# Kernel tuning notes

Hardware: AMD Instinct MI355X
Metric: run time of the kernel (lower is better)

The kernel has to match this reference:

```python
import jax, jax.numpy as jnp
import numpy as np

B, S, W = 32, 256, 32
T = 16               # topics per doc, each spanning L = S//T sentences
VOCAB, E, H, D = 400001, 300, 128, 128


def _gru_scan(x, Wih, Whh, bih, bhh, reverse=False):
    """x: [B,S,E] -> (outputs [B,S,H], final hidden [B,H]). Torch GRU cell math."""
    h0 = jnp.zeros((x.shape[0], Whh.shape[1]), x.dtype)
    gi_all = jnp.einsum('bse,ge->bsg', x, Wih) + bih  # precompute input gates [B,S,3H]

    def step(h, gi):
        gh = h @ Whh.T + bhh
        ir, iz, inn = jnp.split(gi, 3, axis=-1)
        hr, hz, hn = jnp.split(gh, 3, axis=-1)
        r = jax.nn.sigmoid(ir + hr)
        z = jax.nn.sigmoid(iz + hz)
        n = jnp.tanh(inn + r * hn)
        h_new = (1.0 - z) * n + z * h
        return h_new, h_new

    hT, hs = jax.lax.scan(step, h0, jnp.swapaxes(gi_all, 0, 1), reverse=reverse)
    return jnp.swapaxes(hs, 0, 1), hT


def setup_inputs() -> dict:
    key = jax.random.key(0)
    ks = jax.random.split(key, 16)
    sc_i = 1.0 / np.sqrt(H)
    L = S // T
    starts = (jnp.arange(T, dtype=jnp.int32) * L + 1)          # 1-based inclusive
    ends = (jnp.arange(T, dtype=jnp.int32) + 1) * L
    tse = jnp.broadcast_to(jnp.stack([starts, ends], axis=-1)[None], (B, T, 2)).astype(jnp.int32)
    return {
        'word_ids': jax.random.randint(ks[0], (B, S, W), 0, VOCAB, dtype=jnp.int32),
        'topic_start_ends': tse,
        'embed_table': jax.random.normal(ks[1], (VOCAB, E), jnp.float32) * 0.6,
        'Wih_f': jax.random.normal(ks[2], (3 * H, E), jnp.float32) * sc_i,
        'Whh_f': jax.random.normal(ks[3], (3 * H, H), jnp.float32) * sc_i,
        'bih_f': jax.random.normal(ks[4], (3 * H,), jnp.float32) * sc_i,
        'bhh_f': jax.random.normal(ks[5], (3 * H,), jnp.float32) * sc_i,
        'Wih_b': jax.random.normal(ks[6], (3 * H, E), jnp.float32) * sc_i,
        'Whh_b': jax.random.normal(ks[7], (3 * H, H), jnp.float32) * sc_i,
        'bih_b': jax.random.normal(ks[8], (3 * H,), jnp.float32) * sc_i,
        'bhh_b': jax.random.normal(ks[9], (3 * H,), jnp.float32) * sc_i,
        'v_attention': jax.random.normal(ks[10], (4 * H, 1), jnp.float32),
        'W_attention': jax.random.normal(ks[11], (4 * H, 4 * H), jnp.float32) * (1.0 / np.sqrt(4 * H)),
        'W1': jax.random.normal(ks[12], (D, 4 * H), jnp.float32) * (1.0 / np.sqrt(4 * H)),
        'b1': jax.random.normal(ks[13], (D,), jnp.float32) * 0.01,
        'W2': jax.random.normal(ks[14], (1, D), jnp.float32) * (1.0 / np.sqrt(D)),
        'b2': jax.random.normal(ks[15], (1,), jnp.float32) * 0.01,
    }


def reference(word_ids, topic_start_ends, embed_table,
              Wih_f, Whh_f, bih_f, bhh_f, Wih_b, Whh_b, bih_b, bhh_b,
              v_attention, W_attention, W1, b1, W2, b2):
    b, s, _ = word_ids.shape
    h = Whh_f.shape[1]
    # --- sent_encoder: gather word embeddings, mean-pool per sentence ---
    sent_emb = jnp.mean(embed_table[word_ids], axis=2)          # [B,S,E]
    # --- doc_encoder: bi-GRU ---
    out_f, hT_f = _gru_scan(sent_emb, Wih_f, Whh_f, bih_f, bhh_f, reverse=False)
    out_b, hT_b = _gru_scan(sent_emb, Wih_b, Whh_b, bih_b, bhh_b, reverse=True)
    sent_rep = jnp.concatenate([out_f, out_b], axis=-1)         # [B,S,2H]
    # faithful to hidden.view(batch_size, 2H) on hidden of shape [2,B,H]
    doc_vec = jnp.stack([hT_f, hT_b], axis=0).reshape(b, 2 * h)
    doc_rep = jnp.broadcast_to(doc_vec[:, None, :], (b, s, 2 * h))
    # topic reps via segment difference of cumulative GRU states (pad trick)
    pad = jnp.pad(sent_rep, ((0, 0), (1, 1), (0, 0)))           # [B,S+2,2H]
    starts = topic_start_ends[:, :, 0]                          # [B,T], 1-based
    ends = topic_start_ends[:, :, 1]

    def gat(idx, lo, hi):
        return jnp.take_along_axis(pad[..., lo:hi], idx[:, :, None], axis=1)
    fwd_part = gat(ends, 0, h) - gat(starts - 1, 0, h)
    bwd_part = gat(starts, h, 2 * h) - gat(ends + 1, h, 2 * h)
    topic_mat = jnp.concatenate([fwd_part, bwd_part], axis=-1)  # [B,T,2H]
    # scatter topic vectors to sentences: topic id = #starts at or before sentence
    sidx = jnp.arange(s, dtype=starts.dtype)
    topic_id = jnp.sum(sidx[None, :, None] >= (starts - 1)[:, None, :], axis=-1) - 1  # [B,S]
    topic_rep = jnp.take_along_axis(topic_mat, topic_id[:, :, None], axis=1)          # [B,S,2H]
    # --- decoder ---
    cat_ds = jnp.concatenate([doc_rep, sent_rep], axis=-1)      # [B,S,4H]
    cat_ts = jnp.concatenate([topic_rep, sent_rep], axis=-1)
    doc_scores = jnp.tanh(cat_ds @ W_attention) @ v_attention   # [B,S,1]
    topic_scores = jnp.tanh(cat_ts @ W_attention) @ v_attention
    doc_w = jax.nn.softmax(doc_scores, axis=1)
    topic_w = jax.nn.softmax(topic_scores, axis=1)
    context = doc_w * doc_rep + topic_w * topic_rep             # [B,S,2H]
    inp = jnp.concatenate([sent_rep, context], axis=-1)         # [B,S,4H]
    hdd = jax.nn.relu(inp @ W1.T + b1)                          # dropout = identity (eval)
    logits = (hdd @ W2.T + b2).squeeze(-1)                      # [B,S]
    return logits
```

## Files before the change

kernel.cpp:

```cpp
#include <hip/hip_runtime.h>
#include <hip/hip_bf16.h>
#include <cstdint>

#define Bk 32
#define Sk 256
#define Wk 32
#define Tk 16
#define Ek 300
#define Hk 128
#define Dk 128
#define NROWS (Bk*Sk)
#define GI_N  (3*Hk*2)

__device__ __forceinline__ float fast_sigmoid(float x) {
    return 1.f / (1.f + __expf(-x));
}
__device__ __forceinline__ float fast_tanh(float x) {
    float ax = fabsf(x);
    float e = __expf(2.f * ax);
    float t = 1.f - 2.f / (1.f + e);
    return copysignf(t, x);
}
__device__ __forceinline__ void barrier_lgkm() {
    asm volatile("s_waitcnt lgkmcnt(0)" ::: "memory");
    __builtin_amdgcn_s_barrier();
}
__device__ __forceinline__ void fma44(const float4& a, const float4& b, float (&c)[4][4]) {
    c[0][0]=fmaf(a.x,b.x,c[0][0]); c[0][1]=fmaf(a.x,b.y,c[0][1]); c[0][2]=fmaf(a.x,b.z,c[0][2]); c[0][3]=fmaf(a.x,b.w,c[0][3]);
    c[1][0]=fmaf(a.y,b.x,c[1][0]); c[1][1]=fmaf(a.y,b.y,c[1][1]); c[1][2]=fmaf(a.y,b.z,c[1][2]); c[1][3]=fmaf(a.y,b.w,c[1][3]);
    c[2][0]=fmaf(a.z,b.x,c[2][0]); c[2][1]=fmaf(a.z,b.y,c[2][1]); c[2][2]=fmaf(a.z,b.z,c[2][2]); c[2][3]=fmaf(a.z,b.w,c[2][3]);
    c[3][0]=fmaf(a.w,b.x,c[3][0]); c[3][1]=fmaf(a.w,b.y,c[3][1]); c[3][2]=fmaf(a.w,b.z,c[3][2]); c[3][3]=fmaf(a.w,b.w,c[3][3]);
}

__global__ __launch_bounds__(256) void pack_kernel(
    const float* __restrict__ Wf, const float* __restrict__ Wb,
    const float* __restrict__ bf, const float* __restrict__ bb,
    const float* __restrict__ W1,
    float* __restrict__ Bgi, float* __restrict__ bias_gi, float* __restrict__ BW1)
{
    int idx = blockIdx.x * 256 + threadIdx.x;
    if (idx < 300 * 768) {
        int k = idx / 768, n = idx % 768;
        Bgi[idx] = (n < 384) ? Wf[n * 300 + k] : Wb[(n - 384) * 300 + k];
    }
    if (idx < 768) bias_gi[idx] = (idx < 384) ? bf[idx] : bb[idx - 384];
    if (idx < 512 * 128) {
        int k = idx >> 7, n = idx & 127;
        BW1[idx] = W1[n * 512 + k];
    }
}

__global__ __launch_bounds__(256) void embed_mean_kernel(
    const int* __restrict__ wids, const float* __restrict__ table,
    float* __restrict__ sent_emb)
{
    int wv = (blockIdx.x << 2) + (threadIdx.x >> 6);
    int lane = threadIdx.x & 63;
    if (wv >= NROWS) return;
    const int* idp = wids + (size_t)wv * Wk;
    float4 a0 = {0,0,0,0}, a1 = {0,0,0,0};
    #pragma unroll 4
    for (int w = 0; w < Wk; ++w) {
        int id = idp[w];
        const float4* r4 = reinterpret_cast<const float4*>(table + (size_t)id * Ek);
        float4 v0 = r4[lane];
        a0.x += v0.x; a0.y += v0.y; a0.z += v0.z; a0.w += v0.w;
        if (lane < 11) {
            float4 v1 = r4[64 + lane];
            a1.x += v1.x; a1.y += v1.y; a1.z += v1.z; a1.w += v1.w;
        }
    }
    const float sc = 1.f / 32.f;
    float4* o4 = reinterpret_cast<float4*>(sent_emb + (size_t)wv * Ek);
    float4 o0 = {a0.x*sc, a0.y*sc, a0.z*sc, a0.w*sc};
    o4[lane] = o0;
    if (lane < 11) {
        float4 o1 = {a1.x*sc, a1.y*sc, a1.z*sc, a1.w*sc};
        o4[64 + lane] = o1;
    }
}

template<bool BIAS, bool RELU>
__global__ __launch_bounds__(256) void gemm_kernel(
    const float* __restrict__ A, const float* __restrict__ B,
    const float* __restrict__ bias, float* __restrict__ C,
    int M, int N, int K)
{
    __shared__ float As[64][68];
    __shared__ float Bs[64][68];
    const int tid = threadIdx.x;
    const int m0 = blockIdx.x * 64;
    const int n0 = blockIdx.y * 64;
    const int tx = tid & 15, ty = tid >> 4;
    const int lr = tid >> 2;
    const int lc = tid & 3;
    float acc[4][4] = {};

    for (int k0 = 0; k0 < K; k0 += 64) {
        #pragma unroll
        for (int i = 0; i < 4; ++i) {
            int kk = lc * 4 + i * 16;
            int gm = m0 + lr;
            int gk = k0 + kk;
            float4 v = {0,0,0,0};
            if (gm < M && gk < K)
                v = *reinterpret_cast<const float4*>(A + (size_t)gm * K + gk);
            As[kk+0][lr] = v.x; As[kk+1][lr] = v.y; As[kk+2][lr] = v.z; As[kk+3][lr] = v.w;
        }
        #pragma unroll
        for (int i = 0; i < 4; ++i) {
            int nn = lc * 4 + i * 16;
            int gk = k0 + lr;
            float4 v = {0,0,0,0};
            if (gk < K)
                v = *reinterpret_cast<const float4*>(B + (size_t)gk * N + n0 + nn);
            *reinterpret_cast<float4*>(&Bs[lr][nn]) = v;
        }
        __syncthreads();
        #pragma unroll 8
        for (int k = 0; k < 64; ++k) {
            float4 av = *reinterpret_cast<const float4*>(&As[k][ty*4]);
            float4 bv = *reinterpret_cast<const float4*>(&Bs[k][tx*4]);
            fma44(av, bv, acc);
        }
        __syncthreads();
    }
    #pragma unroll
    for (int r = 0; r < 4; ++r) {
        int row = m0 + ty * 4 + r;
        if (row < M) {
            float4 v = {acc[r][0], acc[r][1], acc[r][2], acc[r][3]};
            if (BIAS) {
                const float* bp = bias + n0 + tx * 4;
                v.x += bp[0]; v.y += bp[1]; v.z += bp[2]; v.w += bp[3];
            }
            if (RELU) {
                v.x = fmaxf(v.x, 0.f); v.y = fmaxf(v.y, 0.f);
                v.z = fmaxf(v.z, 0.f); v.w = fmaxf(v.w, 0.f);
            }
            *reinterpret_cast<float4*>(C + (size_t)row * N + n0 + tx * 4) = v;
        }
    }
}

__global__ __launch_bounds__(512, 1) void gru_scan_kernel(
    const float* __restrict__ gi,
    const float* __restrict__ Whh_f, const float* __restrict__ Whh_b,
    const float* __restrict__ bhh_f, const float* __restrict__ bhh_b,
    float* __restrict__ sent_rep,
    float* __restrict__ hT)
{
    const int blk = blockIdx.x;
    const int dir = blk >> 5;
    const int b   = blk & 31;
    const int t = threadIdx.x;
    const int lane = t & 63;
    const int w_id = t >> 6;
    const int q = lane >> 4;
    const int m = lane & 15;
    const int j = w_id * 16 + m;
    const float* Whh = dir ? Whh_b : Whh_f;
    const float* bhh = dir ? bhh_b : bhh_f;
    __shared__ float hbufA[144];
    __shared__ float hbufB[144];

    const float* wr0 = Whh + (size_t)j * 128 + 32 * q;
    const float* wr1 = wr0 + 128 * 128;
    const float* wr2 = wr0 + 256 * 128;
    float4 wA0 = *reinterpret_cast<const float4*>(wr0 +  0);
    float4 wA1 = *reinterpret_cast<const float4*>(wr0 +  4);
    float4 wA2 = *reinterpret_cast<const float4*>(wr0 +  8);
    float4 wA3 = *reinterpret_cast<const float4*>(wr0 + 12);
    float4 wA4 = *reinterpret_cast<const float4*>(wr0 + 16);
    float4 wA5 = *reinterpret_cast<const float4*>(wr0 + 20);
    float4 wA6 = *reinterpret_cast<const float4*>(wr0 + 24);
    float4 wA7 = *reinterpret_cast<const float4*>(wr0 + 28);
    float4 wB0 = *reinterpret_cast<const float4*>(wr1 +  0);
    float4 wB1 = *reinterpret_cast<const float4*>(wr1 +  4);
    float4 wB2 = *reinterpret_cast<const float4*>(wr1 +  8);
    float4 wB3 = *reinterpret_cast<const float4*>(wr1 + 12);
    float4 wB4 = *reinterpret_cast<const float4*>(wr1 + 16);
    float4 wB5 = *reinterpret_cast<const float4*>(wr1 + 20);
    float4 wB6 = *reinterpret_cast<const float4*>(wr1 + 24);
    float4 wB7 = *reinterpret_cast<const float4*>(wr1 + 28);
    float4 wC0 = *reinterpret_cast<const float4*>(wr2 +  0);
    float4 wC1 = *reinterpret_cast<const float4*>(wr2 +  4);
    float4 wC2 = *reinterpret_cast<const float4*>(wr2 +  8);
    float4 wC3 = *reinterpret_cast<const float4*>(wr2 + 12);
    float4 wC4 = *reinterpret_cast<const float4*>(wr2 + 16);
    float4 wC5 = *reinterpret_cast<const float4*>(wr2 + 20);
    float4 wC6 = *reinterpret_cast<const float4*>(wr2 + 24);
    float4 wC7 = *reinterpret_cast<const float4*>(wr2 + 28);
    const float br = bhh[j];
    const float bz = bhh[128 + j];
    const float bn = bhh[256 + j];

    if (t < 144) { hbufA[t] = 0.f; hbufB[t] = 0.f; }

    const int ji = 36 * (j >> 5) + (j & 31);
    const float* gbase = gi + (size_t)(b * Sk) * GI_N + dir * 384 + j;
    float hold = 0.f;
    float gir = 0.f, giz = 0.f, gin_ = 0.f;
    {
        const int s0 = dir ? (Sk - 1) : 0;
        const float* gp = gbase + (size_t)s0 * GI_N;
        gir = gp[0]; giz = gp[128]; gin_ = gp[256];
    }
    __syncthreads();

    #define STEP(RD, WR, SEXPR) { \
        const int s = (SEXPR); \
        const float4* hseg = reinterpret_cast<const float4*>(RD) + 9 * q; \
        float pA = 0.f, pB = 0.f, pC = 0.f; \
        { float4 h4; \
          h4 = hseg[0]; \
          pA=fmaf(wA0.x,h4.x,pA); pA=fmaf(wA0.y,h4.y,pA); pA=fmaf(wA0.z,h4.z,pA); pA=fmaf(wA0.w,h4.w,pA); \
          pB=fmaf(wB0.x,h4.x,pB); pB=fmaf(wB0.y,h4.y,pB); pB=fmaf(wB0.z,h4.z,pB); pB=fmaf(wB0.w,h4.w,pB); \
          pC=fmaf(wC0.x,h4.x,pC); pC=fmaf(wC0.y,h4.y,pC); pC=fmaf(wC0.z,h4.z,pC); pC=fmaf(wC0.w,h4.w,pC); \
          h4 = hseg[1]; \
          pA=fmaf(wA1.x,h4.x,pA); pA=fmaf(wA1.y,h4.y,pA); pA=fmaf(wA1.z,h4.z,pA); pA=fmaf(wA1.w,h4.w,pA); \
          pB=fmaf(wB1.x,h4.x,pB); pB=fmaf(wB1.y,h4.y,pB); pB=fmaf(wB1.z,h4.z,pB); pB=fmaf(wB1.w,h4.w,pB); \
          pC=fmaf(wC1.x,h4.x,pC); pC=fmaf(wC1.y,h4.y,pC); pC=fmaf(wC1.z,h4.z,pC); pC=fmaf(wC1.w,h4.w,pC); \
          h4 = hseg[2]; \
          pA=fmaf(wA2.x,h4.x,pA); pA=fmaf(wA2.y,h4.y,pA); pA=fmaf(wA2.z,h4.z,pA); pA=fmaf(wA2.w,h4.w,pA); \
          pB=fmaf(wB2.x,h4.x,pB); pB=fmaf(wB2.y,h4.y,pB); pB=fmaf(wB2.z,h4.z,pB); pB=fmaf(wB2.w,h4.w,pB); \
          pC=fmaf(wC2.x,h4.x,pC); pC=fmaf(wC2.y,h4.y,pC); pC=fmaf(wC2.z,h4.z,pC); pC=fmaf(wC2.w,h4.w,pC); \
          h4 = hseg[3]; \
          pA=fmaf(wA3.x,h4.x,pA); pA=fmaf(wA3.y,h4.y,pA); pA=fmaf(wA3.z,h4.z,pA); pA=fmaf(wA3.w,h4.w,pA); \
          pB=fmaf(wB3.x,h4.x,pB); pB=fmaf(wB3.y,h4.y,pB); pB=fmaf(wB3.z,h4.z,pB); pB=fmaf(wB3.w,h4.w,pB); \
          pC=fmaf(wC3.x,h4.x,pC); pC=fmaf(wC3.y,h4.y,pC); pC=fmaf(wC3.z,h4.z,pC); pC=fmaf(wC3.w,h4.w,pC); \
          h4 = hseg[4]; \
          pA=fmaf(wA4.x,h4.x,pA); pA=fmaf(wA4.y,h4.y,pA); pA=fmaf(wA4.z,h4.z,pA); pA=fmaf(wA4.w,h4.w,pA); \
          pB=fmaf(wB4.x,h4.x,pB); pB=fmaf(wB4.y,h4.y,pB); pB=fmaf(wB4.z,h4.z,pB); pB=fmaf(wB4.w,h4.w,pB); \
          pC=fmaf(wC4.x,h4.x,pC); pC=fmaf(wC4.y,h4.y,pC); pC=fmaf(wC4.z,h4.z,pC); pC=fmaf(wC4.w,h4.w,pC); \
          h4 = hseg[5]; \
          pA=fmaf(wA5.x,h4.x,pA); pA=fmaf(wA5.y,h4.y,pA); pA=fmaf(wA5.z,h4.z,pA); pA=fmaf(wA5.w,h4.w,pA); \
          pB=fmaf(wB5.x,h4.x,pB); pB=fmaf(wB5.y,h4.y,pB); pB=fmaf(wB5.z,h4.z,pB); pB=fmaf(wB5.w,h4.w,pB); \
          pC=fmaf(wC5.x,h4.x,pC); pC=fmaf(wC5.y,h4.y,pC); pC=fmaf(wC5.z,h4.z,pC); pC=fmaf(wC5.w,h4.w,pC); \
          h4 = hseg[6]; \
          pA=fmaf(wA6.x,h4.x,pA); pA=fmaf(wA6.y,h4.y,pA); pA=fmaf(wA6.z,h4.z,pA); pA=fmaf(wA6.w,h4.w,pA); \
          pB=fmaf(wB6.x,h4.x,pB); pB=fmaf(wB6.y,h4.y,pB); pB=fmaf(wB6.z,h4.z,pB); pB=fmaf(wB6.w,h4.w,pB); \
          pC=fmaf(wC6.x,h4.x,pC); pC=fmaf(wC6.y,h4.y,pC); pC=fmaf(wC6.z,h4.z,pC); pC=fmaf(wC6.w,h4.w,pC); \
          h4 = hseg[7]; \
          pA=fmaf(wA7.x,h4.x,pA); pA=fmaf(wA7.y,h4.y,pA); pA=fmaf(wA7.z,h4.z,pA); pA=fmaf(wA7.w,h4.w,pA); \
          pB=fmaf(wB7.x,h4.x,pB); pB=fmaf(wB7.y,h4.y,pB); pB=fmaf(wB7.z,h4.z,pB); pB=fmaf(wB7.w,h4.w,pB); \
          pC=fmaf(wC7.x,h4.x,pC); pC=fmaf(wC7.y,h4.y,pC); pC=fmaf(wC7.z,h4.z,pC); pC=fmaf(wC7.w,h4.w,pC); } \
        pA += __shfl_xor(pA, 16); pA += __shfl_xor(pA, 32); \
        pB += __shfl_xor(pB, 16); pB += __shfl_xor(pB, 32); \
        pC += __shfl_xor(pC, 16); pC += __shfl_xor(pC, 32); \
        if (q == 0) { \
            float r = fast_sigmoid(gir + pA + br); \
            float z = fast_sigmoid(giz + pB + bz); \
            float n = fast_tanh(gin_ + r * (pC + bn)); \
            hold = (1.f - z) * n + z * hold; \
            (WR)[ji] = hold; \
            sent_rep[(size_t)(b * Sk + s) * 256 + dir * 128 + j] = hold; \
            const int sn = dir ? (s > 0 ? s - 1 : 0) : (s + 1 < Sk ? s + 1 : Sk - 1); \
            const float* gp = gbase + (size_t)sn * GI_N; \
            gir = gp[0]; giz = gp[128]; gin_ = gp[256]; \
        } \
        barrier_lgkm(); \
    }

    for (int step = 0; step < Sk; step += 2) {
        STEP(hbufA, hbufB, dir ? (Sk - 1 - step) : step);
        STEP(hbufB, hbufA, dir ? (Sk - 2 - step) : (step + 1));
    }
    #undef STEP

    if (q == 0) hT[dir * 4096 + b * 128 + j] = hold;
}

__device__ __forceinline__ float4 sr_load_guard(const float* sr, int b, int sidx, int j4) {
    if (sidx < 0 || sidx >= Sk) { float4 z = {0,0,0,0}; return z; }
    return reinterpret_cast<const float4*>(sr)[(size_t)(b * Sk + sidx) * 64 + j4];
}
__global__ __launch_bounds__(64) void prep_kernel(
    const int* __restrict__ tse, const float* __restrict__ sent_rep,
    const float* __restrict__ hT, float* __restrict__ dvtm)
{
    const int b = blockIdx.x;
    const int t = blockIdx.y;
    const int j4 = threadIdx.x;
    if (t == 16) {
        int dir = b >> 4;
        int bb = 2 * (b & 15) + (j4 >> 5);
        int jj4 = j4 & 31;
        float4 v = reinterpret_cast<const float4*>(hT)[dir * 1024 + bb * 32 + jj4];
        reinterpret_cast<float4*>(dvtm)[b * 64 + j4] = v;
    } else {
        int st = tse[b * 32 + t * 2];
        int en = tse[b * 32 + t * 2 + 1];
        float4 va, vb;
        if (j4 < 32) {
            va = sr_load_guard(sent_rep, b, en - 1, j4);
            vb = sr_load_guard(sent_rep, b, st - 2, j4);
        } else {
            va = sr_load_guard(sent_rep, b, st - 1, j4);
            vb = sr_load_guard(sent_rep, b, en, j4);
        }
        float4 v = {va.x - vb.x, va.y - vb.y, va.z - vb.z, va.w - vb.w};
        reinterpret_cast<float4*>(dvtm)[(32 + b * 16 + t) * 64 + j4] = v;
    }
}

__global__ __launch_bounds__(256) void scores_kernel(
    const float* __restrict__ SW,
    const float* __restrict__ dptp,
    const float* __restrict__ vatt,
    const int* __restrict__ tse,
    float* __restrict__ dsc, float* __restrict__ tsc)
{
    int row = (blockIdx.x << 2) + (threadIdx.x >> 6);
    int lane = threadIdx.x & 63;
    if (row >= NROWS) return;
    int b = row >> 8, s = row & 255;
    int ti = 0;
    #pragma unroll
    for (int t = 1; t < 16; ++t) ti += (s >= tse[b * 32 + t * 2] - 1) ? 1 : 0;
    const float4* swr = reinterpret_cast<const float4*>(SW + (size_t)row * 512);
    const float4* dpr = reinterpret_cast<const float4*>(dptp + (size_t)b * 512);
    const float4* tpr = reinterpret_cast<const float4*>(dptp + (size_t)(32 + b * 16 + ti) * 512);
    const float4* vv  = reinterpret_cast<const float4*>(vatt);
    float sd = 0.f, st = 0.f;
    #pragma unroll
    for (int q = 0; q < 2; ++q) {
        int i = lane * 2 + q;
        float4 sw = swr[i], dp = dpr[i], tp = tpr[i], v = vv[i];
        sd += fast_tanh(sw.x + dp.x) * v.x + fast_tanh(sw.y + dp.y) * v.y
            + fast_tanh(sw.z + dp.z) * v.z + fast_tanh(sw.w + dp.w) * v.w;
        st += fast_tanh(sw.x + tp.x) * v.x + fast_tanh(sw.y + tp.y) * v.y
            + fast_tanh(sw.z + tp.z) * v.z + fast_tanh(sw.w + tp.w) * v.w;
    }
    #pragma unroll
    for (int off = 32; off; off >>= 1) {
        sd += __shfl_xor(sd, off);
        st += __shfl_xor(st, off);
    }
    if (lane == 0) { dsc[row] = sd; tsc[row] = st; }
}

__global__ __launch_bounds__(256) void softmax_kernel(float* __restrict__ dsc, float* __restrict__ tsc)
{
    const int b = blockIdx.x, sidx = threadIdx.x;
    const int lane = sidx & 63, wid = sidx >> 6;
    __shared__ float rd[4], rt[4];
    float d = dsc[b * Sk + sidx];
    float t = tsc[b * Sk + sidx];
    float md = d, mt = t;
    #pragma unroll
    for (int off = 32; off; off >>= 1) {
        md = fmaxf(md, __shfl_xor(md, off));
        mt = fmaxf(mt, __shfl_xor(mt, off));
    }
    if (lane == 0) { rd[wid] = md; rt[wid] = mt; }
    __syncthreads();
    md = fmaxf(fmaxf(rd[0], rd[1]), fmaxf(rd[2], rd[3]));
    mt = fmaxf(fmaxf(rt[0], rt[1]), fmaxf(rt[2], rt[3]));
    float ed = __expf(d - md), et = __expf(t - mt);
    float sd = ed, stt = et;
    #pragma unroll
    for (int off = 32; off; off >>= 1) {
        sd += __shfl_xor(sd, off);
        stt += __shfl_xor(stt, off);
    }
    __syncthreads();
    if (lane == 0) { rd[wid] = sd; rt[wid] = stt; }
    __syncthreads();
    sd = rd[0] + rd[1] + rd[2] + rd[3];
    stt = rt[0] + rt[1] + rt[2] + rt[3];
    dsc[b * Sk + sidx] = ed / sd;
    tsc[b * Sk + sidx] = et / stt;
}

__global__ __launch_bounds__(128) void build_inp_kernel(
    const float* __restrict__ sent_rep, const float* __restrict__ dvtm,
    const float* __restrict__ dw, const float* __restrict__ tw,
    const int* __restrict__ tse, float* __restrict__ inp)
{
    int row = blockIdx.x;
    int b = row >> 8, s = row & 255;
    int f4c = threadIdx.x;
    float4 v;
    if (f4c < 64) {
        v = reinterpret_cast<const float4*>(sent_rep)[(size_t)row * 64 + f4c];
    } else {
        int ti = 0;
        #pragma unroll
        for (int t = 1; t < 16; ++t) ti += (s >= tse[b * 32 + t * 2] - 1) ? 1 : 0;
        float dwv = dw[row], twv = tw[row];
        int j4 = f4c - 64;
        float4 dv = reinterpret_cast<const float4*>(dvtm)[b * 64 + j4];
        float4 tm = reinterpret_cast<const float4*>(dvtm)[(32 + b * 16 + ti) * 64 + j4];
        v.x = dwv * dv.x + twv * tm.x;
        v.y = dwv * dv.y + twv * tm.y;
        v.z = dwv * dv.z + twv * tm.z;
        v.w = dwv * dv.w + twv * tm.w;
    }
    reinterpret_cast<float4*>(inp)[(size_t)row * 128 + f4c] = v;
}

__global__ __launch_bounds__(256) void logits_kernel(
    const float* __restrict__ hdd, const float* __restrict__ W2,
    const float* __restrict__ b2, float* __restrict__ out)
{
    int row = (blockIdx.x << 2) + (threadIdx.x >> 6);
    int lane = threadIdx.x & 63;
    if (row >= NROWS) return;
    float acc = hdd[(size_t)row * 128 + lane] * W2[lane]
              + hdd[(size_t)row * 128 + 64 + lane] * W2[64 + lane];
    #pragma unroll
    for (int off = 32; off; off >>= 1) acc += __shfl_xor(acc, off);
    if (lane == 0) out[row] = acc + b2[0];
}

extern "C" void kernel_launch(void* const* d_in, const int* in_sizes, int n_in,
                              void* d_out, int out_size, void* d_ws, size_t ws_size,
                              hipStream_t stream)
{
    const int*   wids  = (const int*)d_in[0];
    const int*   tse   = (const int*)d_in[1];
    const float* table = (const float*)d_in[2];
    const float* Wihf  = (const float*)d_in[3];
    const float* Whhf  = (const float*)d_in[4];
    const float* bihf  = (const float*)d_in[5];
    const float* bhhf  = (const float*)d_in[6];
    const float* Wihb  = (const float*)d_in[7];
    const float* Whhb  = (const float*)d_in[8];
    const float* bihb  = (const float*)d_in[9];
    const float* bhhb  = (const float*)d_in[10];
    const float* vatt  = (const float*)d_in[11];
    const float* Watt  = (const float*)d_in[12];
    const float* W1    = (const float*)d_in[13];
    const float* b1    = (const float*)d_in[14];
    const float* W2    = (const float*)d_in[15];
    const float* b2    = (const float*)d_in[16];
    float* ws = (float*)d_ws;
    float* out = (float*)d_out;

    float* sent_emb = ws + 0;
    float* gi       = ws + 2457600;
    float* sent_rep = ws + 8749056;
    float* hT       = ws + 10846208;
    float* dvtm     = ws + 10854400;
    float* dptp     = ws + 10993664;
    float* dsc      = ws + 11272192;
    float* tsc      = ws + 11280384;
    float* Bgi      = ws + 11288576;
    float* bias_gi  = ws + 11518976;
    float* BW1      = ws + 11519744;
    float* SW       = ws + 0;
    float* inp      = ws + 4194304;
    float* hdd      = ws + 0;

    if (ws_size < (size_t)11585280 * sizeof(float)) return;

    pack_kernel<<<900, 256, 0, stream>>>(Wihf, Wihb, bihf, bihb, W1, Bgi, bias_gi, BW1);
    embed_mean_kernel<<<2048, 256, 0, stream>>>(wids, table, sent_emb);
    gemm_kernel<true,false><<<dim3(128, 12), 256, 0, stream>>>(sent_emb, Bgi, bias_gi, gi, NROWS, 768, 300);
    gru_scan_kernel<<<64, 512, 0, stream>>>(gi, Whhf, Whhb, bhhf, bhhb, sent_rep, hT);
    prep_kernel<<<dim3(32, 17), 64, 0, stream>>>(tse, sent_rep, hT, dvtm);
    gemm_kernel<false,false><<<dim3(128, 8), 256, 0, stream>>>(sent_rep, Watt + 256 * 512, nullptr, SW, NROWS, 512, 256);
    gemm_kernel<false,false><<<dim3(9, 8), 256, 0, stream>>>(dvtm, Watt, nullptr, dptp, 544, 512, 256);
    scores_kernel<<<2048, 256, 0, stream>>>(SW, dptp, vatt, tse, dsc, tsc);
    softmax_kernel<<<32, 256, 0, stream>>>(dsc, tsc);
    build_inp_kernel<<<NROWS, 128, 0, stream>>>(sent_rep, dvtm, dsc, tsc, tse, inp);
    gemm_kernel<true,true><<<dim3(128, 2), 256, 0, stream>>>(inp, BW1, b1, hdd, NROWS, 128, 512);
    logits_kernel<<<2048, 256, 0, stream>>>(hdd, W2, b2, out);
}
```

Baseline: 397.2 us.

## Move input-gate and attention GEMMs to bf16 MFMA with split-precision operands

Replaces the FP32 SIMT GEMM for the GRU input gates with an MFMA bf16 kernel that uses a hi/lo split (three MFMA passes) to keep near-FP32 accuracy. The embedding-mean kernel now writes padded bf16 hi/lo rows directly, and the pack kernel produces transposed bf16 weights. The sentence-side attention GEMM runs as a single-pass bf16 MFMA after a new conversion kernel turns sent_rep into bf16. This trades extra conversion kernels, a larger workspace and reduced precision on the attention projection for matrix-core throughput.

Result: faster. 345.6 us (-13.0%).

```diff
diff --git a/kernel.cpp b/kernel.cpp
--- a/kernel.cpp
+++ b/kernel.cpp
@@ -11,6 +11,10 @@
 #define Dk 128
 #define NROWS (Bk*Sk)
 #define GI_N  (3*Hk*2)
+#define KPAD  320
+
+typedef __attribute__((ext_vector_type(8))) short short8v;
+typedef __attribute__((ext_vector_type(4))) float f32x4;
 
 __device__ __forceinline__ float fast_sigmoid(float x) {
     return 1.f / (1.f + __expf(-x));
@@ -31,19 +35,37 @@
     c[2][0]=fmaf(a.z,b.x,c[2][0]); c[2][1]=fmaf(a.z,b.y,c[2][1]); c[2][2]=fmaf(a.z,b.z,c[2][2]); c[2][3]=fmaf(a.z,b.w,c[2][3]);
     c[3][0]=fmaf(a.w,b.x,c[3][0]); c[3][1]=fmaf(a.w,b.y,c[3][1]); c[3][2]=fmaf(a.w,b.z,c[3][2]); c[3][3]=fmaf(a.w,b.w,c[3][3]);
 }
+__device__ __forceinline__ unsigned short f2bf(float f) {
+    uint32_t u = __float_as_uint(f);
+    uint32_t r = (u + 0x7FFFu + ((u >> 16) & 1u)) >> 16;
+    return (unsigned short)r;
+}
+__device__ __forceinline__ float bf2f(unsigned short h) {
+    return __uint_as_float(((uint32_t)h) << 16);
+}
 
 __global__ __launch_bounds__(256) void pack_kernel(
     const float* __restrict__ Wf, const float* __restrict__ Wb,
     const float* __restrict__ bf, const float* __restrict__ bb,
-    const float* __restrict__ W1,
-    float* __restrict__ Bgi, float* __restrict__ bias_gi, float* __restrict__ BW1)
+    const float* __restrict__ Watt, const float* __restrict__ W1,
+    unsigned short* __restrict__ Bgt_hi, unsigned short* __restrict__ Bgt_lo,
+    float* __restrict__ bias_gi, unsigned short* __restrict__ Wswt,
+    float* __restrict__ BW1)
 {
     int idx = blockIdx.x * 256 + threadIdx.x;
-    if (idx < 300 * 768) {
-        int k = idx / 768, n = idx % 768;
-        Bgi[idx] = (n < 384) ? Wf[n * 300 + k] : Wb[(n - 384) * 300 + k];
+    if (idx < 768 * KPAD) {
+        int n = idx / KPAD, k = idx % KPAD;
+        float v = 0.f;
+        if (k < 300) v = (n < 384) ? Wf[n * 300 + k] : Wb[(n - 384) * 300 + k];
+        unsigned short h = f2bf(v);
+        Bgt_hi[idx] = h;
+        Bgt_lo[idx] = f2bf(v - bf2f(h));
     }
     if (idx < 768) bias_gi[idx] = (idx < 384) ? bf[idx] : bb[idx - 384];
+    if (idx < 512 * 256) {
+        int n = idx >> 8, k = idx & 255;
+        Wswt[idx] = f2bf(Watt[(size_t)(256 + k) * 512 + n]);
+    }
     if (idx < 512 * 128) {
         int k = idx >> 7, n = idx & 127;
         BW1[idx] = W1[n * 512 + k];
@@ -52,7 +74,7 @@
 
 __global__ __launch_bounds__(256) void embed_mean_kernel(
     const int* __restrict__ wids, const float* __restrict__ table,
-    float* __restrict__ sent_emb)
+    unsigned short* __restrict__ Ahi, unsigned short* __restrict__ Alo)
 {
     int wv = (blockIdx.x << 2) + (threadIdx.x >> 6);
     int lane = threadIdx.x & 63;
@@ -71,12 +93,120 @@
         }
     }
     const float sc = 1.f / 32.f;
-    float4* o4 = reinterpret_cast<float4*>(sent_emb + (size_t)wv * Ek);
-    float4 o0 = {a0.x*sc, a0.y*sc, a0.z*sc, a0.w*sc};
-    o4[lane] = o0;
+    unsigned short* hp = Ahi + (size_t)wv * KPAD;
+    unsigned short* lp = Alo + (size_t)wv * KPAD;
+    {
+        float v[4] = {a0.x*sc, a0.y*sc, a0.z*sc, a0.w*sc};
+        ushort4 h, l;
+        h.x=f2bf(v[0]); h.y=f2bf(v[1]); h.z=f2bf(v[2]); h.w=f2bf(v[3]);
+        l.x=f2bf(v[0]-bf2f(h.x)); l.y=f2bf(v[1]-bf2f(h.y));
+        l.z=f2bf(v[2]-bf2f(h.z)); l.w=f2bf(v[3]-bf2f(h.w));
+        *reinterpret_cast<ushort4*>(hp + lane*4) = h;
+        *reinterpret_cast<ushort4*>(lp + lane*4) = l;
+    }
     if (lane < 11) {
-        float4 o1 = {a1.x*sc, a1.y*sc, a1.z*sc, a1.w*sc};
-        o4[64 + lane] = o1;
+        float v[4] = {a1.x*sc, a1.y*sc, a1.z*sc, a1.w*sc};
+        ushort4 h, l;
+        h.x=f2bf(v[0]); h.y=f2bf(v[1]); h.z=f2bf(v[2]); h.w=f2bf(v[3]);
+        l.x=f2bf(v[0]-bf2f(h.x)); l.y=f2bf(v[1]-bf2f(h.y));
+        l.z=f2bf(v[2]-bf2f(h.z)); l.w=f2bf(v[3]-bf2f(h.w));
+        *reinterpret_cast<ushort4*>(hp + 256 + lane*4) = h;
+        *reinterpret_cast<ushort4*>(lp + 256 + lane*4) = l;
+    } else if (lane < 16) {
+        ushort4 z = {0,0,0,0};
+        *reinterpret_cast<ushort4*>(hp + 256 + lane*4) = z;
+        *reinterpret_cast<ushort4*>(lp + 256 + lane*4) = z;
+    }
+}
+
+__global__ __launch_bounds__(256) void cvt_bf16_kernel(
+    const float* __restrict__ src, unsigned short* __restrict__ dst, int n8)
+{
+    int i = blockIdx.x * 256 + threadIdx.x;
+    if (i >= n8) return;
+    const float4* s = reinterpret_cast<const float4*>(src) + (size_t)i * 2;
+    float4 v0 = s[0], v1 = s[1];
+    unsigned short r[8];
+    r[0]=f2bf(v0.x); r[1]=f2bf(v0.y); r[2]=f2bf(v0.z); r[3]=f2bf(v0.w);
+    r[4]=f2bf(v1.x); r[5]=f2bf(v1.y); r[6]=f2bf(v1.z); r[7]=f2bf(v1.w);
+    *reinterpret_cast<short8v*>(dst + (size_t)i * 8) = *reinterpret_cast<short8v*>(r);
+}
+
+template<int PASSES, bool BIAS>
+__global__ __launch_bounds__(256) void mfma_gemm_kernel(
+    const unsigned short* __restrict__ Ahi, const unsigned short* __restrict__ Alo,
+    const unsigned short* __restrict__ Bthi, const unsigned short* __restrict__ Btlo,
+    const float* __restrict__ bias, float* __restrict__ C,
+    int M, int N, int Kp)
+{
+    __shared__ unsigned short At_h[128][40];
+    __shared__ unsigned short Bt_h[128][40];
+    __shared__ unsigned short At_l[128][40];
+    __shared__ unsigned short Bt_l[128][40];
+    const int tid = threadIdx.x;
+    const int m0 = blockIdx.x * 128, n0 = blockIdx.y * 128;
+    const int lane = tid & 63;
+    const int wave = tid >> 6;
+    const int wr = (wave >> 1) * 64, wc = (wave & 1) * 64;
+    const int l15 = lane & 15, l4 = lane >> 4;
+    f32x4 acc[4][4] = {};
+
+    const int srow = tid >> 1;
+    const int scol = (tid & 1) * 16;
+
+    for (int k0 = 0; k0 < Kp; k0 += 32) {
+        {
+            const unsigned short* ag = Ahi + (size_t)(m0 + srow) * Kp + k0 + scol;
+            *reinterpret_cast<short8v*>(&At_h[srow][scol])     = *reinterpret_cast<const short8v*>(ag);
+            *reinterpret_cast<short8v*>(&At_h[srow][scol + 8]) = *reinterpret_cast<const short8v*>(ag + 8);
+            const unsigned short* bg = Bthi + (size_t)(n0 + srow) * Kp + k0 + scol;
+            *reinterpret_cast<short8v*>(&Bt_h[srow][scol])     = *reinterpret_cast<const short8v*>(bg);
+            *reinterpret_cast<short8v*>(&Bt_h[srow][scol + 8]) = *reinterpret_cast<const short8v*>(bg + 8);
+            if (PASSES > 1) {
+                const unsigned short* ag2 = Alo + (size_t)(m0 + srow) * Kp + k0 + scol;
+                *reinterpret_cast<short8v*>(&At_l[srow][scol])     = *reinterpret_cast<const short8v*>(ag2);
+                *reinterpret_cast<short8v*>(&At_l[srow][scol + 8]) = *reinterpret_cast<const short8v*>(ag2 + 8);
+                const unsigned short* bg2 = Btlo + (size_t)(n0 + srow) * Kp + k0 + scol;
+                *reinterpret_cast<short8v*>(&Bt_l[srow][scol])     = *reinterpret_cast<const short8v*>(bg2);
+                *reinterpret_cast<short8v*>(&Bt_l[srow][scol + 8]) = *reinterpret_cast<const short8v*>(bg2 + 8);
+            }
+        }
+        __syncthreads();
+        short8v a_h[4], b_h[4], a_l[4], b_l[4];
+        #pragma unroll
+        for (int f = 0; f < 4; ++f) {
+            a_h[f] = *reinterpret_cast<const short8v*>(&At_h[wr + f*16 + l15][l4*8]);
+            b_h[f] = *reinterpret_cast<const short8v*>(&Bt_h[wc + f*16 + l15][l4*8]);
+            if (PASSES > 1) {
+                a_l[f] = *reinterpret_cast<const short8v*>(&At_l[wr + f*16 + l15][l4*8]);
+                b_l[f] = *reinterpret_cast<const short8v*>(&Bt_l[wc + f*16 + l15][l4*8]);
+            }
+        }
+        #pragma unroll
+        for (int i = 0; i < 4; ++i) {
+            #pragma unroll
+            for (int j = 0; j < 4; ++j) {
+                acc[i][j] = __builtin_amdgcn_mfma_f32_16x16x32_bf16(a_h[i], b_h[j], acc[i][j], 0, 0, 0);
+                if (PASSES > 1) {
+                    acc[i][j] = __builtin_amdgcn_mfma_f32_16x16x32_bf16(a_l[i], b_h[j], acc[i][j], 0, 0, 0);
+                    acc[i][j] = __builtin_amdgcn_mfma_f32_16x16x32_bf16(a_h[i], b_l[j], acc[i][j], 0, 0, 0);
+                }
+            }
+        }
+        __syncthreads();
+    }
+    #pragma unroll
+    for (int i = 0; i < 4; ++i) {
+        #pragma unroll
+        for (int j = 0; j < 4; ++j) {
+            int col = n0 + wc + j * 16 + l15;
+            float badd = BIAS ? bias[col] : 0.f;
+            #pragma unroll
+            for (int r = 0; r < 4; ++r) {
+                int row = m0 + wr + i * 16 + l4 * 4 + r;
+                C[(size_t)row * N + col] = acc[i][j][r] + badd;
+            }
+        }
     }
 }
 
@@ -438,29 +568,37 @@
     float* ws = (float*)d_ws;
     float* out = (float*)d_out;
 
-    float* sent_emb = ws + 0;
-    float* gi       = ws + 2457600;
-    float* sent_rep = ws + 8749056;
-    float* hT       = ws + 10846208;
-    float* dvtm     = ws + 10854400;
-    float* dptp     = ws + 10993664;
-    float* dsc      = ws + 11272192;
-    float* tsc      = ws + 11280384;
-    float* Bgi      = ws + 11288576;
-    float* bias_gi  = ws + 11518976;
-    float* BW1      = ws + 11519744;
-    float* SW       = ws + 0;
-    float* inp      = ws + 4194304;
-    float* hdd      = ws + 0;
-
-    if (ws_size < (size_t)11585280 * sizeof(float)) return;
-
-    pack_kernel<<<900, 256, 0, stream>>>(Wihf, Wihb, bihf, bihb, W1, Bgi, bias_gi, BW1);
-    embed_mean_kernel<<<2048, 256, 0, stream>>>(wids, table, sent_emb);
-    gemm_kernel<true,false><<<dim3(128, 12), 256, 0, stream>>>(sent_emb, Bgi, bias_gi, gi, NROWS, 768, 300);
+    unsigned short* Ahi   = (unsigned short*)(ws + 0);
+    unsigned short* Alo   = (unsigned short*)(ws + 1310720);
+    float* gi             = ws + 2621440;
+    float* sent_rep       = ws + 8912896;
+    unsigned short* SRhi  = (unsigned short*)(ws + 11010048);
+    float* hT             = ws + 12058624;
+    float* dvtm           = ws + 12066816;
+    float* dptp           = ws + 12206080;
+    float* dsc            = ws + 12484608;
+    float* tsc            = ws + 12492800;
+    unsigned short* BgtH  = (unsigned short*)(ws + 12500992);
+    unsigned short* BgtL  = (unsigned short*)(ws + 12623872);
+    float* bias_gi        = ws + 12746752;
+    unsigned short* Wswt  = (unsigned short*)(ws + 12747520);
+    float* BW1            = ws + 12813056;
+    float* SW             = ws + 12878592;
+    float* inp            = ws + 0;
+    float* hdd            = ws + 4194304;
+
+    if (ws_size < (size_t)17072896 * sizeof(float)) return;
+
+    pack_kernel<<<960, 256, 0, stream>>>(Wihf, Wihb, bihf, bihb, Watt, W1,
+                                         BgtH, BgtL, bias_gi, Wswt, BW1);
+    embed_mean_kernel<<<2048, 256, 0, stream>>>(wids, table, Ahi, Alo);
+    mfma_gemm_kernel<3, true><<<dim3(64, 6), 256, 0, stream>>>(
+        Ahi, Alo, BgtH, BgtL, bias_gi, gi, NROWS, 768, KPAD);
     gru_scan_kernel<<<64, 512, 0, stream>>>(gi, Whhf, Whhb, bhhf, bhhb, sent_rep, hT);
+    cvt_bf16_kernel<<<1024, 256, 0, stream>>>(sent_rep, SRhi, NROWS * 256 / 8);
     prep_kernel<<<dim3(32, 17), 64, 0, stream>>>(tse, sent_rep, hT, dvtm);
-    gemm_kernel<false,false><<<dim3(128, 8), 256, 0, stream>>>(sent_rep, Watt + 256 * 512, nullptr, SW, NROWS, 512, 256);
+    mfma_gemm_kernel<1, false><<<dim3(64, 4), 256, 0, stream>>>(
+        SRhi, nullptr, Wswt, nullptr, nullptr, SW, NROWS, 512, 256);
     gemm_kernel<false,false><<<dim3(9, 8), 256, 0, stream>>>(dvtm, Watt, nullptr, dptp, 544, 512, 256);
     scores_kernel<<<2048, 256, 0, stream>>>(SW, dptp, vatt, tse, dsc, tsc);
     softmax_kernel<<<32, 256, 0, stream>>>(dsc, tsc);
```
